# Kernel optimization log

Measured on AMD Instinct MI355X. Metric: run time of the kernel, lower is better.

## Reference

```python
import jax, jax.numpy as jnp
import numpy as np

B, N, M, K = 2, 50000, 50000, 16
C_IN, C_ADD, C_MID = 64, 3, 16


def setup_inputs() -> dict:
    key = jax.random.key(0)
    k1, k2, k3, k4 = jax.random.split(key, 4)
    return {
        "input_features": jax.random.normal(k1, (B, N, C_IN), dtype=jnp.float32),
        "neighbor_inds": jax.random.randint(k2, (B, M, K), 0, N, dtype=jnp.int64),
        "weightnet": jax.random.normal(k3, (B, M, K, C_MID), dtype=jnp.float32),
        "additional_features": jax.random.normal(k4, (B, M, K, C_ADD), dtype=jnp.float32),
    }


def reference(input_features, neighbor_inds, weightnet, additional_features):
    # Gather neighbor features: [B, M, K, C_in]
    gathered = jax.vmap(lambda feat, idx: feat[idx])(input_features, neighbor_inds)
    # Concatenate additional per-neighbor features: [B, M, K, C_in + C_add]
    cat = jnp.concatenate([gathered, additional_features], axis=-1)
    # Weighted reduce over neighbors: [B, M, C_total, C_mid]
    out = jnp.einsum("bmkc,bmkw->bmcw", cat, weightnet)
    b, m = out.shape[:2]
    return out.reshape(b, m, -1)
```

## Files before the change

kernel.cpp:

```cpp
#include <hip/hip_runtime.h>
#include <cstdint>
#include <cstddef>


namespace {
constexpr int B_   = 2;
constexpr int N_   = 50000;
constexpr int M_   = 50000;
constexpr int KNB  = 16;
constexpr int CIN  = 64;
constexpr int COUT = 67 * 16;
constexpr int PAIRS = B_ * M_;
constexpr int FELEMS = B_ * N_ * CIN;
}

typedef unsigned int u32;
typedef float  f32x4  __attribute__((ext_vector_type(4)));
typedef short  short8 __attribute__((ext_vector_type(8)));
typedef u32    u32x4  __attribute__((ext_vector_type(4)));
typedef u32    u32x2  __attribute__((ext_vector_type(2)));

struct IdxS   { int v[16]; };
struct StageT { unsigned short bg[4][8]; float ad[8]; float wf[8]; };
struct StageF { float bg[4][8]; float ad[8]; float wf[8]; };

static __device__ __forceinline__ short8 pack_bf8(const float* x) {
  u32x4 w;
  #pragma unroll
  for (int q = 0; q < 4; ++q)
    w[q] = __builtin_amdgcn_perm(__builtin_bit_cast(u32, x[2*q+1]),
                                 __builtin_bit_cast(u32, x[2*q]),
                                 0x07060302u);
  return __builtin_bit_cast(short8, w);
}

static __device__ __forceinline__ u32 bfrne(float x) {
  u32 u = __builtin_bit_cast(u32, x);
  return (u + 0x7FFFu + ((u >> 16) & 1u)) >> 16;
}

__global__ __launch_bounds__(256)
void cvt_feat_bf16(const float* __restrict__ src, unsigned short* __restrict__ dst) {
  const int n4 = FELEMS / 4;
  int i = blockIdx.x * blockDim.x + threadIdx.x;
  const int stride = gridDim.x * blockDim.x;
  const f32x4* s4 = reinterpret_cast<const f32x4*>(src);
  for (; i < n4; i += stride) {
    f32x4 v = s4[i];
    u32x2 w;
    w[0] = bfrne(v[0]) | (bfrne(v[1]) << 16);
    w[1] = bfrne(v[2]) | (bfrne(v[3]) << 16);
    *reinterpret_cast<u32x2*>(dst + 4 * (size_t)i) = w;
  }
}

static __device__ __forceinline__ void load_idx(const int* __restrict__ idxp, IdxS& r) {
  #pragma unroll
  for (int j = 0; j < 16; ++j)
    r.v[j] = __builtin_amdgcn_readfirstlane(idxp[j]);
}

static __device__ __forceinline__ void load_stage_t(const unsigned short* __restrict__ fb,
                                                    const float* __restrict__ wnp,
                                                    const float* __restrict__ adp,
                                                    const IdxS& I, int lane, StageT& S) {
  const int cc = lane & 15;
  if (lane < 32) {
    const int hi = lane >> 4;
    int rows[8];
    #pragma unroll
    for (int j = 0; j < 8; ++j) rows[j] = hi ? I.v[j + 8] : I.v[j];
    #pragma unroll
    for (int j = 0; j < 8; ++j) {
      const u32 rb = ((u32)rows[j]) << 6;
      #pragma unroll
      for (int t = 0; t < 4; ++t)
        S.bg[t][j] = fb[rb + (u32)(t * 16 + cc)];
    }
    const u32 woff = (hi ? 128u : 0u) + (u32)cc;
    #pragma unroll
    for (int j = 0; j < 8; ++j)
      S.wf[j] = __builtin_nontemporal_load(wnp + woff + j * 16);
    if (cc < 3) {
      const u32 aoff = (hi ? 24u : 0u) + (u32)cc;
      #pragma unroll
      for (int j = 0; j < 8; ++j)
        S.ad[j] = __builtin_nontemporal_load(adp + aoff + j * 3);
    }
  }
}

static __device__ __forceinline__ void compute_store_t(const StageT& S,
                                                       float* __restrict__ op, int lane) {
  const int cc = lane & 15, g = lane >> 4;
  const int soff = cc * 16 + g * 4;
  const short8 a = pack_bf8(S.wf);
  #pragma unroll
  for (int t = 0; t < 4; ++t) {
    short8 b;
    #pragma unroll
    for (int j = 0; j < 8; ++j) b[j] = (short)S.bg[t][j];
    f32x4 acc = {0.f, 0.f, 0.f, 0.f};
    acc = __builtin_amdgcn_mfma_f32_16x16x32_bf16(a, b, acc, 0, 0, 0);
    __builtin_nontemporal_store(acc, reinterpret_cast<f32x4*>(op + soff + t * 256));
  }
  {
    const short8 b = pack_bf8(S.ad);
    f32x4 acc = {0.f, 0.f, 0.f, 0.f};
    acc = __builtin_amdgcn_mfma_f32_16x16x32_bf16(a, b, acc, 0, 0, 0);
    if (cc < 3)
      __builtin_nontemporal_store(acc, reinterpret_cast<f32x4*>(op + soff + 1024));
  }
}

__global__ __launch_bounds__(256, 4)
void pconv7_tbl(const unsigned short* __restrict__ tbl, const int* __restrict__ inds,
                const float* __restrict__ wnet, const float* __restrict__ addf,
                float* __restrict__ out)
{
  const int lane = threadIdx.x & 63;
  const int gw = __builtin_amdgcn_readfirstlane(
      (int)((blockIdx.x * blockDim.x + threadIdx.x) >> 6));
  const int nw = (int)((gridDim.x * blockDim.x) >> 6);
  if (gw >= PAIRS) return;

  IdxS iCur, iNext;
  load_idx(inds + (size_t)gw * KNB, iCur);

  for (int p = gw; p < PAIRS; p += nw) {
    const int pn = (p + nw < PAIRS) ? (p + nw) : gw;
    load_idx(inds + (size_t)pn * KNB, iNext);
    const int b = p / M_;
    StageT S = {};
    load_stage_t(tbl + (size_t)b * N_ * CIN, wnet + (size_t)p * 256,
                 addf + (size_t)p * 48, iCur, lane, S);
    compute_store_t(S, out + (size_t)p * COUT, lane);
    #pragma unroll
    for (int j = 0; j < 16; ++j) iCur.v[j] = iNext.v[j];
  }
}

static __device__ __forceinline__ void load_stage_f(const float* __restrict__ fb,
                                                    const float* __restrict__ wnp,
                                                    const float* __restrict__ adp,
                                                    const IdxS& I, int lane, StageF& S) {
  const int cc = lane & 15;
  if (lane < 32) {
    const int hi = lane >> 4;
    int rows[8];
    #pragma unroll
    for (int j = 0; j < 8; ++j) rows[j] = hi ? I.v[j + 8] : I.v[j];
    #pragma unroll
    for (int j = 0; j < 8; ++j) {
      const u32 rb = ((u32)rows[j]) << 6;
      #pragma unroll
      for (int t = 0; t < 4; ++t)
        S.bg[t][j] = fb[rb + (u32)(t * 16 + cc)];
    }
    const u32 woff = (hi ? 128u : 0u) + (u32)cc;
    #pragma unroll
    for (int j = 0; j < 8; ++j)
      S.wf[j] = __builtin_nontemporal_load(wnp + woff + j * 16);
    if (cc < 3) {
      const u32 aoff = (hi ? 24u : 0u) + (u32)cc;
      #pragma unroll
      for (int j = 0; j < 8; ++j)
        S.ad[j] = __builtin_nontemporal_load(adp + aoff + j * 3);
    }
  }
}

static __device__ __forceinline__ void compute_store_f(const StageF& S,
                                                       float* __restrict__ op, int lane) {
  const int cc = lane & 15, g = lane >> 4;
  const int soff = cc * 16 + g * 4;
  const short8 a = pack_bf8(S.wf);
  #pragma unroll
  for (int t = 0; t < 4; ++t) {
    const short8 b = pack_bf8(S.bg[t]);
    f32x4 acc = {0.f, 0.f, 0.f, 0.f};
    acc = __builtin_amdgcn_mfma_f32_16x16x32_bf16(a, b, acc, 0, 0, 0);
    __builtin_nontemporal_store(acc, reinterpret_cast<f32x4*>(op + soff + t * 256));
  }
  {
    const short8 b = pack_bf8(S.ad);
    f32x4 acc = {0.f, 0.f, 0.f, 0.f};
    acc = __builtin_amdgcn_mfma_f32_16x16x32_bf16(a, b, acc, 0, 0, 0);
    if (cc < 3)
      __builtin_nontemporal_store(acc, reinterpret_cast<f32x4*>(op + soff + 1024));
  }
}

__global__ __launch_bounds__(256, 4)
void pconv7_f32(const float* __restrict__ feat, const int* __restrict__ inds,
                const float* __restrict__ wnet, const float* __restrict__ addf,
                float* __restrict__ out)
{
  const int lane = threadIdx.x & 63;
  const int gw = __builtin_amdgcn_readfirstlane(
      (int)((blockIdx.x * blockDim.x + threadIdx.x) >> 6));
  const int nw = (int)((gridDim.x * blockDim.x) >> 6);
  if (gw >= PAIRS) return;

  IdxS iCur, iNext;
  load_idx(inds + (size_t)gw * KNB, iCur);

  for (int p = gw; p < PAIRS; p += nw) {
    const int pn = (p + nw < PAIRS) ? (p + nw) : gw;
    load_idx(inds + (size_t)pn * KNB, iNext);
    const int b = p / M_;
    StageF S = {};
    load_stage_f(feat + (size_t)b * N_ * CIN, wnet + (size_t)p * 256,
                 addf + (size_t)p * 48, iCur, lane, S);
    compute_store_f(S, out + (size_t)p * COUT, lane);
    #pragma unroll
    for (int j = 0; j < 16; ++j) iCur.v[j] = iNext.v[j];
  }
}

extern "C" void kernel_launch(void* const* d_in, const int* in_sizes, int n_in,
                              void* d_out, int out_size, void* d_ws, size_t ws_size,
                              hipStream_t stream) {
  const float* feat = (const float*)d_in[0];
  const int*   inds = (const int*)d_in[1];
  const float* wnet = (const float*)d_in[2];
  const float* addf = (const float*)d_in[3];
  float* outp = (float*)d_out;

  const size_t TBL_BYTES = (size_t)FELEMS * sizeof(unsigned short);

  dim3 grid(4096), block(256);
  if (ws_size >= TBL_BYTES) {
    unsigned short* tbl = (unsigned short*)d_ws;
    hipLaunchKernelGGL(cvt_feat_bf16, dim3(2048), dim3(256), 0, stream, feat, tbl);
    hipLaunchKernelGGL(pconv7_tbl, grid, block, 0, stream,
                       tbl, inds, wnet, addf, outp);
  } else {
    hipLaunchKernelGGL(pconv7_f32, grid, block, 0, stream,
                       feat, inds, wnet, addf, outp);
  }
}
```

Before: 162.6 us.

## Use all 64 lanes with 16x16x16 bf16 MFMA per neighbor pair

Replaces the bf16-table kernel with a variant where all four 16-lane groups each gather four neighbors and weights. Each group feeds the K=16 MFMA (16x16x16bf16_1k), where before only half the wavefront did loads for a K=32 MFMA. This spreads the gather and load latency across the whole wave, cuts per-lane register state, and raises the occupancy hint to 8 blocks per CU. It also replaces the batch division with a comparison. The old path is kept only as a fallback when the builtin is unavailable.

```diff
diff --git a/kernel.cpp b/kernel.cpp
--- a/kernel.cpp
+++ b/kernel.cpp
@@ -15,13 +15,13 @@
 }
 
 typedef unsigned int u32;
-typedef float  f32x4  __attribute__((ext_vector_type(4)));
-typedef short  short8 __attribute__((ext_vector_type(8)));
-typedef u32    u32x4  __attribute__((ext_vector_type(4)));
-typedef u32    u32x2  __attribute__((ext_vector_type(2)));
+typedef float  f32x4   __attribute__((ext_vector_type(4)));
+typedef short  short8  __attribute__((ext_vector_type(8)));
+typedef short  short4v __attribute__((ext_vector_type(4)));
+typedef u32    u32x4   __attribute__((ext_vector_type(4)));
+typedef u32    u32x2   __attribute__((ext_vector_type(2)));
 
 struct IdxS   { int v[16]; };
-struct StageT { unsigned short bg[4][8]; float ad[8]; float wf[8]; };
 struct StageF { float bg[4][8]; float ad[8]; float wf[8]; };
 
 static __device__ __forceinline__ short8 pack_bf8(const float* x) {
@@ -32,6 +32,16 @@
                                  __builtin_bit_cast(u32, x[2*q]),
                                  0x07060302u);
   return __builtin_bit_cast(short8, w);
+}
+
+static __device__ __forceinline__ short4v pack_bf4(const float* x) {
+  u32x2 w;
+  #pragma unroll
+  for (int q = 0; q < 2; ++q)
+    w[q] = __builtin_amdgcn_perm(__builtin_bit_cast(u32, x[2*q+1]),
+                                 __builtin_bit_cast(u32, x[2*q]),
+                                 0x07060302u);
+  return __builtin_bit_cast(short4v, w);
 }
 
 static __device__ __forceinline__ u32 bfrne(float x) {
@@ -60,6 +70,93 @@
     r.v[j] = __builtin_amdgcn_readfirstlane(idxp[j]);
 }
 
+#if __has_builtin(__builtin_amdgcn_mfma_f32_16x16x16bf16_1k)
+
+__global__ __launch_bounds__(256, 8)
+void pconv10(const unsigned short* __restrict__ tbl, const int* __restrict__ inds,
+             const float* __restrict__ wnet, const float* __restrict__ addf,
+             float* __restrict__ out)
+{
+  const int lane = threadIdx.x & 63;
+  const int cc = lane & 15, g = lane >> 4;
+  const int g1 = g & 1, g2 = g >> 1;
+  const int gw = __builtin_amdgcn_readfirstlane(
+      (int)((blockIdx.x * blockDim.x + threadIdx.x) >> 6));
+  const int nw = (int)((gridDim.x * blockDim.x) >> 6);
+  if (gw >= PAIRS) return;
+
+  IdxS iCur, iNext;
+  load_idx(inds + (size_t)gw * KNB, iCur);
+
+  for (int p = gw; p < PAIRS; p += nw) {
+    const int pn = (p + nw < PAIRS) ? (p + nw) : gw;
+    load_idx(inds + (size_t)pn * KNB, iNext);
+
+    const int b = (p >= M_) ? 1 : 0;
+    const unsigned short* __restrict__ fb  = tbl + (size_t)b * N_ * CIN;
+    const float* __restrict__ wnp = wnet + (size_t)p * 256;
+    const float* __restrict__ adp = addf + (size_t)p * 48;
+
+    int row[4];
+    #pragma unroll
+    for (int j = 0; j < 4; ++j) {
+      const int ra = g1 ? iCur.v[4 + j]  : iCur.v[j];
+      const int rb = g1 ? iCur.v[12 + j] : iCur.v[8 + j];
+      row[j] = g2 ? rb : ra;
+    }
+
+    u32 bg[4][4];
+    #pragma unroll
+    for (int j = 0; j < 4; ++j) {
+      const unsigned short* __restrict__ rp = fb + (((u32)row[j]) << 6) + (u32)cc;
+      #pragma unroll
+      for (int t = 0; t < 4; ++t)
+        bg[t][j] = rp[t * 16];
+    }
+
+    float wf[4];
+    const float* __restrict__ wp = wnp + g * 64 + cc;
+    #pragma unroll
+    for (int j = 0; j < 4; ++j)
+      wf[j] = __builtin_nontemporal_load(wp + j * 16);
+
+    float ad[4];
+    const float* __restrict__ ap = adp + g * 12 + cc;
+    #pragma unroll
+    for (int j = 0; j < 4; ++j)
+      ad[j] = (cc < 3) ? __builtin_nontemporal_load(ap + j * 3) : 0.f;
+
+    const short4v a = pack_bf4(wf);
+    float* __restrict__ op = out + (size_t)p * COUT;
+    const int soff = cc * 16 + g * 4;
+
+    #pragma unroll
+    for (int t = 0; t < 4; ++t) {
+      u32x2 w;
+      w[0] = bg[t][0] | (bg[t][1] << 16);
+      w[1] = bg[t][2] | (bg[t][3] << 16);
+      const short4v bb = __builtin_bit_cast(short4v, w);
+      f32x4 acc = {0.f, 0.f, 0.f, 0.f};
+      acc = __builtin_amdgcn_mfma_f32_16x16x16bf16_1k(a, bb, acc, 0, 0, 0);
+      __builtin_nontemporal_store(acc, reinterpret_cast<f32x4*>(op + soff + t * 256));
+    }
+    {
+      const short4v bb = pack_bf4(ad);
+      f32x4 acc = {0.f, 0.f, 0.f, 0.f};
+      acc = __builtin_amdgcn_mfma_f32_16x16x16bf16_1k(a, bb, acc, 0, 0, 0);
+      if (cc < 3)
+        __builtin_nontemporal_store(acc, reinterpret_cast<f32x4*>(op + soff + 1024));
+    }
+
+    #pragma unroll
+    for (int j = 0; j < 16; ++j) iCur.v[j] = iNext.v[j];
+  }
+}
+
+#else
+
+struct StageT { unsigned short bg[4][8]; float ad[8]; float wf[8]; };
+
 static __device__ __forceinline__ void load_stage_t(const unsigned short* __restrict__ fb,
                                                     const float* __restrict__ wnp,
                                                     const float* __restrict__ adp,
@@ -90,33 +187,10 @@
   }
 }
 
-static __device__ __forceinline__ void compute_store_t(const StageT& S,
-                                                       float* __restrict__ op, int lane) {
-  const int cc = lane & 15, g = lane >> 4;
-  const int soff = cc * 16 + g * 4;
-  const short8 a = pack_bf8(S.wf);
-  #pragma unroll
-  for (int t = 0; t < 4; ++t) {
-    short8 b;
-    #pragma unroll
-    for (int j = 0; j < 8; ++j) b[j] = (short)S.bg[t][j];
-    f32x4 acc = {0.f, 0.f, 0.f, 0.f};
-    acc = __builtin_amdgcn_mfma_f32_16x16x32_bf16(a, b, acc, 0, 0, 0);
-    __builtin_nontemporal_store(acc, reinterpret_cast<f32x4*>(op + soff + t * 256));
-  }
-  {
-    const short8 b = pack_bf8(S.ad);
-    f32x4 acc = {0.f, 0.f, 0.f, 0.f};
-    acc = __builtin_amdgcn_mfma_f32_16x16x32_bf16(a, b, acc, 0, 0, 0);
-    if (cc < 3)
-      __builtin_nontemporal_store(acc, reinterpret_cast<f32x4*>(op + soff + 1024));
-  }
-}
-
 __global__ __launch_bounds__(256, 4)
-void pconv7_tbl(const unsigned short* __restrict__ tbl, const int* __restrict__ inds,
-                const float* __restrict__ wnet, const float* __restrict__ addf,
-                float* __restrict__ out)
+void pconv10(const unsigned short* __restrict__ tbl, const int* __restrict__ inds,
+             const float* __restrict__ wnet, const float* __restrict__ addf,
+             float* __restrict__ out)
 {
   const int lane = threadIdx.x & 63;
   const int gw = __builtin_amdgcn_readfirstlane(
@@ -126,19 +200,39 @@
 
   IdxS iCur, iNext;
   load_idx(inds + (size_t)gw * KNB, iCur);
-
   for (int p = gw; p < PAIRS; p += nw) {
     const int pn = (p + nw < PAIRS) ? (p + nw) : gw;
     load_idx(inds + (size_t)pn * KNB, iNext);
-    const int b = p / M_;
+    const int b = (p >= M_) ? 1 : 0;
     StageT S = {};
     load_stage_t(tbl + (size_t)b * N_ * CIN, wnet + (size_t)p * 256,
                  addf + (size_t)p * 48, iCur, lane, S);
-    compute_store_t(S, out + (size_t)p * COUT, lane);
+    const int cc = lane & 15, g = lane >> 4;
+    const int soff = cc * 16 + g * 4;
+    float* op = out + (size_t)p * COUT;
+    const short8 a = pack_bf8(S.wf);
+    #pragma unroll
+    for (int t = 0; t < 4; ++t) {
+      short8 bb;
+      #pragma unroll
+      for (int j = 0; j < 8; ++j) bb[j] = (short)S.bg[t][j];
+      f32x4 acc = {0.f, 0.f, 0.f, 0.f};
+      acc = __builtin_amdgcn_mfma_f32_16x16x32_bf16(a, bb, acc, 0, 0, 0);
+      __builtin_nontemporal_store(acc, reinterpret_cast<f32x4*>(op + soff + t * 256));
+    }
+    {
+      const short8 bb = pack_bf8(S.ad);
+      f32x4 acc = {0.f, 0.f, 0.f, 0.f};
+      acc = __builtin_amdgcn_mfma_f32_16x16x32_bf16(a, bb, acc, 0, 0, 0);
+      if (cc < 3)
+        __builtin_nontemporal_store(acc, reinterpret_cast<f32x4*>(op + soff + 1024));
+    }
     #pragma unroll
     for (int j = 0; j < 16; ++j) iCur.v[j] = iNext.v[j];
   }
 }
+
+#endif
 
 static __device__ __forceinline__ void load_stage_f(const float* __restrict__ fb,
                                                     const float* __restrict__ wnp,
@@ -170,31 +264,10 @@
   }
 }
 
-static __device__ __forceinline__ void compute_store_f(const StageF& S,
-                                                       float* __restrict__ op, int lane) {
-  const int cc = lane & 15, g = lane >> 4;
-  const int soff = cc * 16 + g * 4;
-  const short8 a = pack_bf8(S.wf);
-  #pragma unroll
-  for (int t = 0; t < 4; ++t) {
-    const short8 b = pack_bf8(S.bg[t]);
-    f32x4 acc = {0.f, 0.f, 0.f, 0.f};
-    acc = __builtin_amdgcn_mfma_f32_16x16x32_bf16(a, b, acc, 0, 0, 0);
-    __builtin_nontemporal_store(acc, reinterpret_cast<f32x4*>(op + soff + t * 256));
-  }
-  {
-    const short8 b = pack_bf8(S.ad);
-    f32x4 acc = {0.f, 0.f, 0.f, 0.f};
-    acc = __builtin_amdgcn_mfma_f32_16x16x32_bf16(a, b, acc, 0, 0, 0);
-    if (cc < 3)
-      __builtin_nontemporal_store(acc, reinterpret_cast<f32x4*>(op + soff + 1024));
-  }
-}
-
 __global__ __launch_bounds__(256, 4)
-void pconv7_f32(const float* __restrict__ feat, const int* __restrict__ inds,
-                const float* __restrict__ wnet, const float* __restrict__ addf,
-                float* __restrict__ out)
+void pconv10_f32(const float* __restrict__ feat, const int* __restrict__ inds,
+                 const float* __restrict__ wnet, const float* __restrict__ addf,
+                 float* __restrict__ out)
 {
   const int lane = threadIdx.x & 63;
   const int gw = __builtin_amdgcn_readfirstlane(
@@ -204,15 +277,31 @@
 
   IdxS iCur, iNext;
   load_idx(inds + (size_t)gw * KNB, iCur);
-
   for (int p = gw; p < PAIRS; p += nw) {
     const int pn = (p + nw < PAIRS) ? (p + nw) : gw;
     load_idx(inds + (size_t)pn * KNB, iNext);
-    const int b = p / M_;
+    const int b = (p >= M_) ? 1 : 0;
     StageF S = {};
     load_stage_f(feat + (size_t)b * N_ * CIN, wnet + (size_t)p * 256,
                  addf + (size_t)p * 48, iCur, lane, S);
-    compute_store_f(S, out + (size_t)p * COUT, lane);
+    const int cc = lane & 15, g = lane >> 4;
+    const int soff = cc * 16 + g * 4;
+    float* op = out + (size_t)p * COUT;
+    const short8 a = pack_bf8(S.wf);
+    #pragma unroll
+    for (int t = 0; t < 4; ++t) {
+      const short8 bb = pack_bf8(S.bg[t]);
+      f32x4 acc = {0.f, 0.f, 0.f, 0.f};
+      acc = __builtin_amdgcn_mfma_f32_16x16x32_bf16(a, bb, acc, 0, 0, 0);
+      __builtin_nontemporal_store(acc, reinterpret_cast<f32x4*>(op + soff + t * 256));
+    }
+    {
+      const short8 bb = pack_bf8(S.ad);
+      f32x4 acc = {0.f, 0.f, 0.f, 0.f};
+      acc = __builtin_amdgcn_mfma_f32_16x16x32_bf16(a, bb, acc, 0, 0, 0);
+      if (cc < 3)
+        __builtin_nontemporal_store(acc, reinterpret_cast<f32x4*>(op + soff + 1024));
+    }
     #pragma unroll
     for (int j = 0; j < 16; ++j) iCur.v[j] = iNext.v[j];
   }
@@ -233,10 +322,9 @@
   if (ws_size >= TBL_BYTES) {
     unsigned short* tbl = (unsigned short*)d_ws;
     hipLaunchKernelGGL(cvt_feat_bf16, dim3(2048), dim3(256), 0, stream, feat, tbl);
-    hipLaunchKernelGGL(pconv7_tbl, grid, block, 0, stream,
-                       tbl, inds, wnet, addf, outp);
+    hipLaunchKernelGGL(pconv10, grid, block, 0, stream, tbl, inds, wnet, addf, outp);
   } else {
-    hipLaunchKernelGGL(pconv7_f32, grid, block, 0, stream,
+    hipLaunchKernelGGL(pconv10_f32, grid, block, 0, stream,
                        feat, inds, wnet, addf, outp);
   }
 }
```

Result: slower. 166.1 us (+2.2%).
